# Performance work log

Measured on AMD Instinct MI355X. Metric: run time of the kernel, lower is better.

The kernel has to match this reference:

```python
import jax, jax.numpy as jnp
import numpy as np

MARGIN = 0.3
K_AN = 3
K_AP = 6
KMAX = max(K_AN, K_AP)
NORMALIZE = True


def setup_inputs() -> dict:
    key = jax.random.key(0)
    k1, k2 = jax.random.split(key)
    inputs = jax.random.normal(k1, (128, 32, 128), dtype=jnp.float32)
    targets = jax.random.randint(k2, (128,), 0, 16, dtype=jnp.int64)
    return {"inputs": inputs, "targets": targets}


def _pair_stats(xi, xj):
    # xi, xj: (s, d) L2-normalized features of two tracklets
    s = xi.shape[0]
    xc = jnp.concatenate([xi, xj], axis=0)                     # (m, d), m = 2s
    sq = jnp.sum(xc * xc, axis=1)                              # (m,)
    dist = sq[:, None] + sq[None, :] - 2.0 * (xc @ xc.T)       # (m, m)
    dist = jnp.sqrt(jnp.clip(dist, 1e-12))
    # softmax over full m x m, THEN slice the cross block [0:s, s:m]
    row = jax.nn.softmax(dist, axis=1)[:s, s:]                 # (s, s)
    col = jax.nn.softmax(dist, axis=0)[:s, s:]                 # (s, s)
    a = jnp.min(row, axis=1)                                   # (s,) per-row mins
    c = jnp.min(col, axis=0)                                   # (s,) per-col mins
    ta = jax.lax.top_k(a, KMAX)[0]                             # sorted descending
    tc = jax.lax.top_k(c, KMAX)[0]
    v_same = jnp.maximum(ta[K_AP - 1], tc[K_AP - 1])           # k_ap-th largest
    v_diff = jnp.minimum(ta[K_AN - 1], tc[K_AN - 1])           # k_an-th largest
    return v_same, v_diff


def _loss(inputs, targets):
    b = inputs.shape[0]
    x = inputs
    if NORMALIZE:
        nrm = jnp.linalg.norm(x, axis=-1, keepdims=True)
        x = x / jnp.clip(nrm, 1e-12)
    # all-pairs stats: (b, b) each
    v_same, v_diff = jax.vmap(lambda xi: jax.vmap(lambda xj: _pair_stats(xi, xj))(x))(x)
    mask = targets[:, None] == targets[None, :]
    D = jnp.where(mask, v_same, v_diff)
    eye = jnp.eye(b, dtype=bool)
    D = jnp.where(eye, 0.0, D)                                 # torch loop leaves diag = 0
    dist_ap = jnp.max(jnp.where(mask, D, -jnp.inf), axis=1)    # hardest positive (incl. diag 0)
    dist_an = jnp.min(jnp.where(mask, jnp.inf, D), axis=1)     # hardest negative
    # MarginRankingLoss(margin)(an, ap, y=1) = mean(relu(ap - an + margin))
    return jnp.mean(jax.nn.relu(dist_ap - dist_an + MARGIN))


def reference(inputs, targets):
    return _loss(inputs, targets)
```

## Files before the change

### kernel.cpp

```cpp
#include <hip/hip_runtime.h>
#include <math.h>

#define B 128
#define S 32
#define Dm 128
#define NV (B * S)
#define MARGINF 0.3f
#define NBLK 2080

typedef __attribute__((ext_vector_type(8))) short short8;
typedef __attribute__((ext_vector_type(16))) float f32x16;

#define GLOBAL_AS __attribute__((address_space(1)))
#define LDS_AS __attribute__((address_space(3)))

#define FSQRT(x) __builtin_amdgcn_sqrtf(x)
#define FEXP(x) __expf(x)

__device__ inline unsigned short f2bf(float f) {
    unsigned u = __float_as_uint(f);
    unsigned r = u + 0x7FFF + ((u >> 16) & 1);
    return (unsigned short)(r >> 16);
}
__device__ inline float bf2f(unsigned short h) {
    return __uint_as_float(((unsigned)h) << 16);
}

__global__ __launch_bounds__(256) void prep_kernel(const float* __restrict__ X,
                                                   unsigned short* __restrict__ Zn,
                                                   float* __restrict__ sqv,
                                                   float* __restrict__ diagsum) {
    int i = blockIdx.x;
    __shared__ unsigned short zlds[4096];
    __shared__ float sq_sh[32];
    int t = threadIdx.x;

    int v = t >> 3;
    int s = t & 7;
    const float4* row = (const float4*)(X + (((size_t)i * S + v) << 7));

    float4 f[4];
    float ss = 0.f;
#pragma unroll
    for (int k = 0; k < 4; ++k) {
        f[k] = row[k * 8 + s];
        ss += f[k].x * f[k].x + f[k].y * f[k].y + f[k].z * f[k].z + f[k].w * f[k].w;
    }
    ss += __shfl_xor(ss, 1); ss += __shfl_xor(ss, 2); ss += __shfl_xor(ss, 4);
    float inv = 1.0f / fmaxf(FSQRT(ss), 1e-12f);

    float s2 = 0.f;
    unsigned short* zrow = Zn + (((size_t)i * S + v) << 7);
#pragma unroll
    for (int k = 0; k < 4; ++k) {
        int fidx = k * 8 + s;
        ushort4 h;
        h.x = f2bf(f[k].x * inv); h.y = f2bf(f[k].y * inv);
        h.z = f2bf(f[k].z * inv); h.w = f2bf(f[k].w * inv);
        float gx = bf2f(h.x), gy = bf2f(h.y), gz = bf2f(h.z), gw = bf2f(h.w);
        s2 += gx * gx + gy * gy + gz * gz + gw * gw;
        *(ushort4*)(zrow + fidx * 4) = h;
        int addr = (v << 8) + ((((fidx >> 1) ^ (v & 7))) << 4) + ((fidx & 1) << 3);
        *(ushort4*)((char*)zlds + addr) = h;
    }
    s2 += __shfl_xor(s2, 1); s2 += __shfl_xor(s2, 2); s2 += __shfl_xor(s2, 4);
    if (s == 0) { sqv[(i << 5) + v] = s2; sq_sh[v] = s2; }
    __syncthreads();

    if (t < 64) {
        int lq = t & 31, kh = t >> 5, sx = lq & 7;
        f32x16 acc;
#pragma unroll
        for (int r = 0; r < 16; ++r) acc[r] = 0.f;
#pragma unroll
        for (int ks = 0; ks < 8; ++ks) {
            int off = (lq << 8) + (((2 * ks + kh) ^ sx) << 4);
            short8 av = *(const short8*)((char*)zlds + off);
            acc = __builtin_amdgcn_mfma_f32_32x32x16_bf16(av, av, acc, 0, 0, 0);
        }
        float sql = sq_sh[lq];
        float ssum = 0.f;
#pragma unroll
        for (int r = 0; r < 16; ++r) {
            int m = (r & 3) + 8 * (r >> 2) + 4 * kh;
            float d2 = sq_sh[m] + sql - 2.f * acc[r];
            ssum += FEXP(FSQRT(fmaxf(d2, 1e-12f)));
        }
        ssum += __shfl_xor(ssum, 32);
        if (t < 32) diagsum[(i << 5) + lq] = ssum;
    }
}

__global__ __launch_bounds__(256) void pair_kernel(const unsigned short* __restrict__ Zn,
                                                   const float* __restrict__ sqv,
                                                   const float* __restrict__ diagsum,
                                                   const int* __restrict__ tgt,
                                                   float* __restrict__ Dmat) {
    int t0 = blockIdx.x;
    int jg = (int)((sqrtf(8.f * (float)t0 + 1.f) - 1.f) * 0.25f);
    while (jg > 0 && t0 < 2 * jg * jg + jg) --jg;
    while (t0 >= 2 * (jg + 1) * (jg + 1) + (jg + 1)) ++jg;
    int i = t0 - (2 * jg * jg + jg);
    int jbase = jg * 4;

    extern __shared__ unsigned short lds[];

    int t = threadIdx.x;
    int w = t >> 6;
    int lane = t & 63;

    {
        int slot = lane & 15;
        int rhi = lane >> 4;
#pragma unroll
        for (int k = 0; k < 10; ++k) {
            int seg = w * 10 + k;
            int panel = seg >> 3;
            int row = ((seg & 7) << 2) | rhi;
            int vec = (panel == 0) ? i : (jbase + panel - 1);
            const unsigned short* gsrc =
                Zn + ((size_t)vec << 12) + (row << 7) + ((slot ^ (row & 7)) << 3);
            unsigned short* ldst = lds + seg * 512;
            __builtin_amdgcn_global_load_lds((const GLOBAL_AS void*)(const void*)gsrc,
                                             (LDS_AS void*)(void*)ldst, 16, 0, 0);
        }
    }
    __syncthreads();

    int j = jbase + w;
    if (j <= i) return;

    const unsigned short* Pi = lds;
    const unsigned short* Pj = lds + (w + 1) * 4096;
    int lq = lane & 31;
    int kh = lane >> 5;
    int sx = lq & 7;

    f32x16 acc, acc2;
#pragma unroll
    for (int r = 0; r < 16; ++r) { acc[r] = 0.f; acc2[r] = 0.f; }

#pragma unroll
    for (int ks = 0; ks < 8; ++ks) {
        int off = (lq << 7) + (((2 * ks + kh) ^ sx) << 3);
        short8 av = *(const short8*)(Pi + off);
        short8 bv = *(const short8*)(Pj + off);
        acc  = __builtin_amdgcn_mfma_f32_32x32x16_bf16(av, bv, acc, 0, 0, 0);
        acc2 = __builtin_amdgcn_mfma_f32_32x32x16_bf16(bv, av, acc2, 0, 0, 0);
    }

    float sqi_l = sqv[(i << 5) + lq];
    float sqj_l = sqv[(j << 5) + lq];
    float di = diagsum[(i << 5) + lq];
    float dj = diagsum[(j << 5) + lq];

    float csum = 0.f, cmin = INFINITY, rsum = 0.f, rmin = INFINITY;
#pragma unroll
    for (int r = 0; r < 16; ++r) {
        int m = (r & 3) + 8 * (r >> 2) + 4 * kh;
        float sqim = __shfl(sqi_l, m);
        float sqjm = __shfl(sqj_l, m);
        float d2a = sqim + sqj_l - 2.f * acc[r];
        float ea = FEXP(FSQRT(fmaxf(d2a, 1e-12f)));
        csum += ea; cmin = fminf(cmin, ea);
        float d2b = sqi_l + sqjm - 2.f * acc2[r];
        float eb = FEXP(FSQRT(fmaxf(d2b, 1e-12f)));
        rsum += eb; rmin = fminf(rmin, eb);
    }
    csum += __shfl_xor(csum, 32);
    cmin = fminf(cmin, __shfl_xor(cmin, 32));
    rsum += __shfl_xor(rsum, 32);
    rmin = fminf(rmin, __shfl_xor(rmin, 32));

    float aval = rmin / (di + rsum);
    float cval = cmin / (dj + csum);

    float v = (lane < 32) ? aval : cval;
#pragma unroll
    for (int k = 2; k <= 32; k <<= 1) {
#pragma unroll
        for (int mm = k >> 1; mm >= 1; mm >>= 1) {
            float o = __shfl_xor(v, mm);
            bool asc = ((lq & k) == 0);
            bool upper = (lq & mm) != 0;
            float mn = fminf(v, o), mx = fmaxf(v, o);
            v = (asc == upper) ? mx : mn;
        }
    }
    float ta3 = __shfl(v, 29), ta6 = __shfl(v, 26);
    float tc3 = __shfl(v, 61), tc6 = __shfl(v, 58);

    if (lane == 0) {
        float v_same = fmaxf(ta6, tc6);
        float v_diff = fminf(ta3, tc3);
        float val = (tgt[i] == tgt[j]) ? v_same : v_diff;
        Dmat[i * B + j] = val;
        Dmat[j * B + i] = val;
    }
}

__global__ __launch_bounds__(128) void final_kernel(const float* __restrict__ Dmat,
                                                    const int* __restrict__ tgt,
                                                    float* __restrict__ out) {
    int i = threadIdx.x;
    int ti = tgt[i];
    float ap = -INFINITY, an = INFINITY;
    for (int jj = 0; jj < B; ++jj) {
        float v = (jj == i) ? 0.f : Dmat[i * B + jj];
        if (tgt[jj] == ti) ap = fmaxf(ap, v);
        else an = fminf(an, v);
    }
    float term = ap - an + MARGINF;
    term = term > 0.f ? term : 0.f;

    __shared__ float red[128];
    red[i] = term;
    __syncthreads();
    for (int off = 64; off >= 1; off >>= 1) {
        if (i < off) red[i] += red[i + off];
        __syncthreads();
    }
    if (i == 0) out[0] = red[0] / (float)B;
}

extern "C" void kernel_launch(void* const* d_in, const int* in_sizes, int n_in,
                              void* d_out, int out_size, void* d_ws, size_t ws_size,
                              hipStream_t stream) {
    const float* X = (const float*)d_in[0];
    const int* tgt = (const int*)d_in[1];
    float* out = (float*)d_out;

    unsigned short* Zn = (unsigned short*)d_ws;
    float* sqv = (float*)(Zn + (size_t)NV * Dm);
    float* diagsum = sqv + NV;
    float* Dmat = diagsum + NV;

    prep_kernel<<<B, 256, 0, stream>>>(X, Zn, sqv, diagsum);
    pair_kernel<<<NBLK, 256, 5 * 4096 * sizeof(unsigned short), stream>>>(
        Zn, sqv, diagsum, tgt, Dmat);
    final_kernel<<<1, 128, 0, stream>>>(Dmat, tgt, out);
}
```

Before: 35.61 us.

## Tile pair kernel into 4x4 tracklet blocks to reuse LDS panels

Replaces the 1x4 row-strip block mapping (2080 blocks, many with idle waves on the triangle edge) with a triangular grid of 4x4 tracklet tiles (528 blocks). Each block loads 8 panels, or 4 on diagonal tiles, and each wave loops over up to 4 pairs. This raises panel reuse, cuts redundant global loads and avoids waves that exit early. In exchange, each block does more serial work, uses more LDS, and diagonal tiles have uneven per-wave load (2 vs 1 pairs).

```diff
diff --git a/kernel.cpp b/kernel.cpp
--- a/kernel.cpp
+++ b/kernel.cpp
@@ -6,7 +6,8 @@
 #define Dm 128
 #define NV (B * S)
 #define MARGINF 0.3f
-#define NBLK 2080
+#define NGRP 32
+#define NBLK (NGRP * (NGRP + 1) / 2)
 
 typedef __attribute__((ext_vector_type(8))) short short8;
 typedef __attribute__((ext_vector_type(16))) float f32x16;
@@ -97,27 +98,28 @@
                                                    const int* __restrict__ tgt,
                                                    float* __restrict__ Dmat) {
     int t0 = blockIdx.x;
-    int jg = (int)((sqrtf(8.f * (float)t0 + 1.f) - 1.f) * 0.25f);
-    while (jg > 0 && t0 < 2 * jg * jg + jg) --jg;
-    while (t0 >= 2 * (jg + 1) * (jg + 1) + (jg + 1)) ++jg;
-    int i = t0 - (2 * jg * jg + jg);
-    int jbase = jg * 4;
+    int jg = (int)((sqrtf(8.f * (float)t0 + 1.f) - 1.f) * 0.5f);
+    while (jg > 0 && t0 < jg * (jg + 1) / 2) --jg;
+    while (t0 >= (jg + 1) * (jg + 2) / 2) ++jg;
+    int ig = t0 - jg * (jg + 1) / 2;
 
     extern __shared__ unsigned short lds[];
 
     int t = threadIdx.x;
     int w = t >> 6;
     int lane = t & 63;
+    bool diagb = (ig == jg);
 
     {
+        int npan = diagb ? 4 : 8;
+        int per = npan * 2;
         int slot = lane & 15;
         int rhi = lane >> 4;
-#pragma unroll
-        for (int k = 0; k < 10; ++k) {
-            int seg = w * 10 + k;
+        for (int k = 0; k < per; ++k) {
+            int seg = w * per + k;
             int panel = seg >> 3;
             int row = ((seg & 7) << 2) | rhi;
-            int vec = (panel == 0) ? i : (jbase + panel - 1);
+            int vec = (panel < 4) ? (ig * 4 + panel) : (jg * 4 + (panel - 4));
             const unsigned short* gsrc =
                 Zn + ((size_t)vec << 12) + (row << 7) + ((slot ^ (row & 7)) << 3);
             unsigned short* ldst = lds + seg * 512;
@@ -127,75 +129,86 @@
     }
     __syncthreads();
 
-    int j = jbase + w;
-    if (j <= i) return;
-
-    const unsigned short* Pi = lds;
-    const unsigned short* Pj = lds + (w + 1) * 4096;
     int lq = lane & 31;
     int kh = lane >> 5;
     int sx = lq & 7;
 
-    f32x16 acc, acc2;
-#pragma unroll
-    for (int r = 0; r < 16; ++r) { acc[r] = 0.f; acc2[r] = 0.f; }
-
-#pragma unroll
-    for (int ks = 0; ks < 8; ++ks) {
-        int off = (lq << 7) + (((2 * ks + kh) ^ sx) << 3);
-        short8 av = *(const short8*)(Pi + off);
-        short8 bv = *(const short8*)(Pj + off);
-        acc  = __builtin_amdgcn_mfma_f32_32x32x16_bf16(av, bv, acc, 0, 0, 0);
-        acc2 = __builtin_amdgcn_mfma_f32_32x32x16_bf16(bv, av, acc2, 0, 0, 0);
-    }
-
-    float sqi_l = sqv[(i << 5) + lq];
-    float sqj_l = sqv[(j << 5) + lq];
-    float di = diagsum[(i << 5) + lq];
-    float dj = diagsum[(j << 5) + lq];
-
-    float csum = 0.f, cmin = INFINITY, rsum = 0.f, rmin = INFINITY;
-#pragma unroll
-    for (int r = 0; r < 16; ++r) {
-        int m = (r & 3) + 8 * (r >> 2) + 4 * kh;
-        float sqim = __shfl(sqi_l, m);
-        float sqjm = __shfl(sqj_l, m);
-        float d2a = sqim + sqj_l - 2.f * acc[r];
-        float ea = FEXP(FSQRT(fmaxf(d2a, 1e-12f)));
-        csum += ea; cmin = fminf(cmin, ea);
-        float d2b = sqi_l + sqjm - 2.f * acc2[r];
-        float eb = FEXP(FSQRT(fmaxf(d2b, 1e-12f)));
-        rsum += eb; rmin = fminf(rmin, eb);
-    }
-    csum += __shfl_xor(csum, 32);
-    cmin = fminf(cmin, __shfl_xor(cmin, 32));
-    rsum += __shfl_xor(rsum, 32);
-    rmin = fminf(rmin, __shfl_xor(rmin, 32));
-
-    float aval = rmin / (di + rsum);
-    float cval = cmin / (dj + csum);
-
-    float v = (lane < 32) ? aval : cval;
-#pragma unroll
-    for (int k = 2; k <= 32; k <<= 1) {
-#pragma unroll
-        for (int mm = k >> 1; mm >= 1; mm >>= 1) {
-            float o = __shfl_xor(v, mm);
-            bool asc = ((lq & k) == 0);
-            bool upper = (lq & mm) != 0;
-            float mn = fminf(v, o), mx = fmaxf(v, o);
-            v = (asc == upper) ? mx : mn;
-        }
-    }
-    float ta3 = __shfl(v, 29), ta6 = __shfl(v, 26);
-    float tc3 = __shfl(v, 61), tc6 = __shfl(v, 58);
-
-    if (lane == 0) {
-        float v_same = fmaxf(ta6, tc6);
-        float v_diff = fminf(ta3, tc3);
-        float val = (tgt[i] == tgt[j]) ? v_same : v_diff;
-        Dmat[i * B + j] = val;
-        Dmat[j * B + i] = val;
+    int npairs = diagb ? ((w < 2) ? 2 : 1) : 4;
+    for (int pp = 0; pp < npairs; ++pp) {
+        int i, j, pa, pb;
+        if (diagb) {
+            int idx = w + pp * 4;
+            pa = (idx >= 3) + (idx >= 5);
+            pb = (idx < 3) ? idx + 1 : ((idx < 5) ? idx - 1 : 3);
+            i = ig * 4 + pa; j = ig * 4 + pb;
+        } else {
+            pa = w; pb = 4 + pp;
+            i = ig * 4 + w; j = jg * 4 + pp;
+        }
+        const unsigned short* Pi = lds + pa * 4096;
+        const unsigned short* Pj = lds + pb * 4096;
+
+        f32x16 acc, acc2;
+#pragma unroll
+        for (int r = 0; r < 16; ++r) { acc[r] = 0.f; acc2[r] = 0.f; }
+
+#pragma unroll
+        for (int ks = 0; ks < 8; ++ks) {
+            int off = (lq << 7) + (((2 * ks + kh) ^ sx) << 3);
+            short8 av = *(const short8*)(Pi + off);
+            short8 bv = *(const short8*)(Pj + off);
+            acc  = __builtin_amdgcn_mfma_f32_32x32x16_bf16(av, bv, acc, 0, 0, 0);
+            acc2 = __builtin_amdgcn_mfma_f32_32x32x16_bf16(bv, av, acc2, 0, 0, 0);
+        }
+
+        float sqi_l = sqv[(i << 5) + lq];
+        float sqj_l = sqv[(j << 5) + lq];
+        float di = diagsum[(i << 5) + lq];
+        float dj = diagsum[(j << 5) + lq];
+
+        float csum = 0.f, cmin = INFINITY, rsum = 0.f, rmin = INFINITY;
+#pragma unroll
+        for (int r = 0; r < 16; ++r) {
+            int m = (r & 3) + 8 * (r >> 2) + 4 * kh;
+            float sqim = __shfl(sqi_l, m);
+            float sqjm = __shfl(sqj_l, m);
+            float d2a = sqim + sqj_l - 2.f * acc[r];
+            float ea = FEXP(FSQRT(fmaxf(d2a, 1e-12f)));
+            csum += ea; cmin = fminf(cmin, ea);
+            float d2b = sqi_l + sqjm - 2.f * acc2[r];
+            float eb = FEXP(FSQRT(fmaxf(d2b, 1e-12f)));
+            rsum += eb; rmin = fminf(rmin, eb);
+        }
+        csum += __shfl_xor(csum, 32);
+        cmin = fminf(cmin, __shfl_xor(cmin, 32));
+        rsum += __shfl_xor(rsum, 32);
+        rmin = fminf(rmin, __shfl_xor(rmin, 32));
+
+        float aval = rmin / (di + rsum);
+        float cval = cmin / (dj + csum);
+
+        float v = (lane < 32) ? aval : cval;
+#pragma unroll
+        for (int k = 2; k <= 32; k <<= 1) {
+#pragma unroll
+            for (int mm = k >> 1; mm >= 1; mm >>= 1) {
+                float o = __shfl_xor(v, mm);
+                bool asc = ((lq & k) == 0);
+                bool upper = (lq & mm) != 0;
+                float mn = fminf(v, o), mx = fmaxf(v, o);
+                v = (asc == upper) ? mx : mn;
+            }
+        }
+        float ta3 = __shfl(v, 29), ta6 = __shfl(v, 26);
+        float tc3 = __shfl(v, 61), tc6 = __shfl(v, 58);
+
+        if (lane == 0) {
+            float v_same = fmaxf(ta6, tc6);
+            float v_diff = fminf(ta3, tc3);
+            float val = (tgt[i] == tgt[j]) ? v_same : v_diff;
+            Dmat[i * B + j] = val;
+            Dmat[j * B + i] = val;
+        }
     }
 }
 
@@ -236,7 +249,7 @@
     float* Dmat = diagsum + NV;
 
     prep_kernel<<<B, 256, 0, stream>>>(X, Zn, sqv, diagsum);
-    pair_kernel<<<NBLK, 256, 5 * 4096 * sizeof(unsigned short), stream>>>(
+    pair_kernel<<<NBLK, 256, 8 * 4096 * sizeof(unsigned short), stream>>>(
         Zn, sqv, diagsum, tgt, Dmat);
     final_kernel<<<1, 128, 0, stream>>>(Dmat, tgt, out);
 }
```

New measurement: 40.83 us. 1.15x slower.

## Split each pair's two MFMA directions across two wavefronts per block

Applied to the files above, without the earlier changes.

Doubles the pair kernel's block size to 512 threads so that each (i,j) pair is handled by two waves, one per softmax direction, rather than one wave computing both GEMMs and both exp reductions. The per-direction values are exchanged through LDS with two extra barriers, and the bitonic top-k runs on the second wave. This aims to cut per-wave latency and raise parallelism, in exchange for more waves, extra synchronisation and the same LDS footprint per block, which may reduce how many blocks fit on a CU.

```diff
diff --git a/kernel.cpp b/kernel.cpp
--- a/kernel.cpp
+++ b/kernel.cpp
@@ -91,7 +91,7 @@
     }
 }
 
-__global__ __launch_bounds__(256) void pair_kernel(const unsigned short* __restrict__ Zn,
+__global__ __launch_bounds__(512) void pair_kernel(const unsigned short* __restrict__ Zn,
                                                    const float* __restrict__ sqv,
                                                    const float* __restrict__ diagsum,
                                                    const int* __restrict__ tgt,
@@ -113,8 +113,8 @@
         int slot = lane & 15;
         int rhi = lane >> 4;
 #pragma unroll
-        for (int k = 0; k < 10; ++k) {
-            int seg = w * 10 + k;
+        for (int k = 0; k < 5; ++k) {
+            int seg = w * 5 + k;
             int panel = seg >> 3;
             int row = ((seg & 7) << 2) | rhi;
             int vec = (panel == 0) ? i : (jbase + panel - 1);
@@ -127,75 +127,90 @@
     }
     __syncthreads();
 
-    int j = jbase + w;
-    if (j <= i) return;
-
-    const unsigned short* Pi = lds;
-    const unsigned short* Pj = lds + (w + 1) * 4096;
+    int pw = w >> 1;
+    int h = w & 1;
+    int j = jbase + pw;
+    bool act = (j > i);
     int lq = lane & 31;
     int kh = lane >> 5;
     int sx = lq & 7;
 
-    f32x16 acc, acc2;
-#pragma unroll
-    for (int r = 0; r < 16; ++r) { acc[r] = 0.f; acc2[r] = 0.f; }
-
-#pragma unroll
-    for (int ks = 0; ks < 8; ++ks) {
-        int off = (lq << 7) + (((2 * ks + kh) ^ sx) << 3);
-        short8 av = *(const short8*)(Pi + off);
-        short8 bv = *(const short8*)(Pj + off);
-        acc  = __builtin_amdgcn_mfma_f32_32x32x16_bf16(av, bv, acc, 0, 0, 0);
-        acc2 = __builtin_amdgcn_mfma_f32_32x32x16_bf16(bv, av, acc2, 0, 0, 0);
-    }
-
-    float sqi_l = sqv[(i << 5) + lq];
-    float sqj_l = sqv[(j << 5) + lq];
-    float di = diagsum[(i << 5) + lq];
-    float dj = diagsum[(j << 5) + lq];
-
-    float csum = 0.f, cmin = INFINITY, rsum = 0.f, rmin = INFINITY;
-#pragma unroll
-    for (int r = 0; r < 16; ++r) {
-        int m = (r & 3) + 8 * (r >> 2) + 4 * kh;
-        float sqim = __shfl(sqi_l, m);
-        float sqjm = __shfl(sqj_l, m);
-        float d2a = sqim + sqj_l - 2.f * acc[r];
-        float ea = FEXP(FSQRT(fmaxf(d2a, 1e-12f)));
-        csum += ea; cmin = fminf(cmin, ea);
-        float d2b = sqi_l + sqjm - 2.f * acc2[r];
-        float eb = FEXP(FSQRT(fmaxf(d2b, 1e-12f)));
-        rsum += eb; rmin = fminf(rmin, eb);
-    }
-    csum += __shfl_xor(csum, 32);
-    cmin = fminf(cmin, __shfl_xor(cmin, 32));
-    rsum += __shfl_xor(rsum, 32);
-    rmin = fminf(rmin, __shfl_xor(rmin, 32));
-
-    float aval = rmin / (di + rsum);
-    float cval = cmin / (dj + csum);
-
-    float v = (lane < 32) ? aval : cval;
-#pragma unroll
-    for (int k = 2; k <= 32; k <<= 1) {
-#pragma unroll
-        for (int mm = k >> 1; mm >= 1; mm >>= 1) {
-            float o = __shfl_xor(v, mm);
-            bool asc = ((lq & k) == 0);
-            bool upper = (lq & mm) != 0;
-            float mn = fminf(v, o), mx = fmaxf(v, o);
-            v = (asc == upper) ? mx : mn;
-        }
-    }
-    float ta3 = __shfl(v, 29), ta6 = __shfl(v, 26);
-    float tc3 = __shfl(v, 61), tc6 = __shfl(v, 58);
-
-    if (lane == 0) {
-        float v_same = fmaxf(ta6, tc6);
-        float v_diff = fminf(ta3, tc3);
-        float val = (tgt[i] == tgt[j]) ? v_same : v_diff;
-        Dmat[i * B + j] = val;
-        Dmat[j * B + i] = val;
+    float val01 = 0.f;
+    if (act) {
+        const unsigned short* Pi = lds;
+        const unsigned short* Pj = lds + (pw + 1) * 4096;
+
+        f32x16 acc;
+#pragma unroll
+        for (int r = 0; r < 16; ++r) acc[r] = 0.f;
+
+        if (h == 0) {
+#pragma unroll
+            for (int ks = 0; ks < 8; ++ks) {
+                int off = (lq << 7) + (((2 * ks + kh) ^ sx) << 3);
+                short8 av = *(const short8*)(Pi + off);
+                short8 bv = *(const short8*)(Pj + off);
+                acc = __builtin_amdgcn_mfma_f32_32x32x16_bf16(av, bv, acc, 0, 0, 0);
+            }
+        } else {
+#pragma unroll
+            for (int ks = 0; ks < 8; ++ks) {
+                int off = (lq << 7) + (((2 * ks + kh) ^ sx) << 3);
+                short8 av = *(const short8*)(Pi + off);
+                short8 bv = *(const short8*)(Pj + off);
+                acc = __builtin_amdgcn_mfma_f32_32x32x16_bf16(bv, av, acc, 0, 0, 0);
+            }
+        }
+
+        int own = h ? i : j;
+        int oth = h ? j : i;
+        float sq_own = sqv[(own << 5) + lq];
+        float sq_shf = sqv[(oth << 5) + lq];
+        float dd = diagsum[(own << 5) + lq];
+
+        float ssum = 0.f, smin = INFINITY;
+#pragma unroll
+        for (int r = 0; r < 16; ++r) {
+            int m = (r & 3) + 8 * (r >> 2) + 4 * kh;
+            float sm = __shfl(sq_shf, m);
+            float d2 = sm + sq_own - 2.f * acc[r];
+            float e = FEXP(FSQRT(fmaxf(d2, 1e-12f)));
+            ssum += e; smin = fminf(smin, e);
+        }
+        ssum += __shfl_xor(ssum, 32);
+        smin = fminf(smin, __shfl_xor(smin, 32));
+        val01 = smin / (dd + ssum);
+    }
+
+    __syncthreads();
+    float* exch = (float*)lds;
+    if (act && h == 0 && lane < 32) exch[pw * 32 + lq] = val01;
+    __syncthreads();
+
+    if (act && h == 1) {
+        float v = (lane < 32) ? val01 : exch[pw * 32 + (lane - 32)];
+
+#pragma unroll
+        for (int k = 2; k <= 32; k <<= 1) {
+#pragma unroll
+            for (int mm = k >> 1; mm >= 1; mm >>= 1) {
+                float o = __shfl_xor(v, mm);
+                bool asc = ((lq & k) == 0);
+                bool upper = (lq & mm) != 0;
+                float mn = fminf(v, o), mx = fmaxf(v, o);
+                v = (asc == upper) ? mx : mn;
+            }
+        }
+        float ta3 = __shfl(v, 29), ta6 = __shfl(v, 26);
+        float tc3 = __shfl(v, 61), tc6 = __shfl(v, 58);
+
+        if (lane == 0) {
+            float v_same = fmaxf(ta6, tc6);
+            float v_diff = fminf(ta3, tc3);
+            float val = (tgt[i] == tgt[j]) ? v_same : v_diff;
+            Dmat[i * B + j] = val;
+            Dmat[j * B + i] = val;
+        }
     }
 }
 
@@ -236,7 +251,7 @@
     float* Dmat = diagsum + NV;
 
     prep_kernel<<<B, 256, 0, stream>>>(X, Zn, sqv, diagsum);
-    pair_kernel<<<NBLK, 256, 5 * 4096 * sizeof(unsigned short), stream>>>(
+    pair_kernel<<<NBLK, 512, 5 * 4096 * sizeof(unsigned short), stream>>>(
         Zn, sqv, diagsum, tgt, Dmat);
     final_kernel<<<1, 128, 0, stream>>>(Dmat, tgt, out);
 }
```

After: 41.71 us. 17.1% more time.
